# Kernel optimization log

Hardware: AMD Instinct MI355X
Metric: run time of the kernel (lower is better)

## Reference

```python
import jax, jax.numpy as jnp
import numpy as np

N = 100000        # nodes
E = 1_600_000     # edges (avg degree 16)
IN = 128          # in_feats
HID = 64          # hidden_feats
H = 3             # num_heads
OUT = 16          # out_feats
NEG_SLOPE = 0.2   # DGL GATConv default LeakyReLU slope


def setup_inputs() -> dict:
    key = jax.random.key(0)
    ks = jax.random.split(key, 16)
    f = lambda k, shape, s=0.1: (jax.random.normal(k, shape, jnp.float32) * s)
    return {
        "features": f(ks[0], (N, IN), 1.0),
        "src": jax.random.randint(ks[1], (E,), 0, N),
        "dst": jax.random.randint(ks[2], (E,), 0, N),
        # GATConv 1: in -> (H, HID)
        "W1": f(ks[3], (IN, H * HID)),
        "al1": f(ks[4], (H, HID)),
        "ar1": f(ks[5], (H, HID)),
        "b1": f(ks[6], (H, HID)),
        # GATConv 2: H*HID -> (H, HID)
        "W2": f(ks[7], (H * HID, H * HID)),
        "al2": f(ks[8], (H, HID)),
        "ar2": f(ks[9], (H, HID)),
        "b2": f(ks[10], (H, HID)),
        # MLP head
        "w3": f(ks[11], (H * HID, HID)),
        "b3": f(ks[12], (HID,)),
        "w4": f(ks[13], (HID, OUT)),
        "b4": f(ks[14], (OUT,)),
    }


def gat_layer(x, src, dst, W, al, ar, b):
    # feat: (N, H, D) projected features
    feat = (x @ W).reshape(-1, H, HID)
    el = jnp.einsum('nhd,hd->nh', feat, al)   # (N, H)
    er = jnp.einsum('nhd,hd->nh', feat, ar)   # (N, H)
    e = el[src] + er[dst]                     # (E, H) edge scores
    e = jnp.where(e > 0, e, NEG_SLOPE * e)    # LeakyReLU
    # numerically stable softmax over incoming edges of each dst node
    m = jax.lax.stop_gradient(jax.ops.segment_max(e, dst, num_segments=N))
    ex = jnp.exp(e - m[dst])
    s = jax.ops.segment_sum(ex, dst, num_segments=N)
    alpha = ex / s[dst]                       # (E, H)
    # message passing: scatter alpha-weighted src features to dst
    out = jax.ops.segment_sum(alpha[:, :, None] * feat[src], dst, num_segments=N)
    return jax.nn.relu(out + b)               # (N, H, D)


def reference(features, src, dst, W1, al1, ar1, b1, W2, al2, ar2, b2, w3, b3, w4, b4):
    x = gat_layer(features, src, dst, W1, al1, ar1, b1).reshape(N, H * HID)
    x = gat_layer(x, src, dst, W2, al2, ar2, b2).reshape(N, H * HID)
    h = jax.nn.relu(x @ w3 + b3)
    return h @ w4 + b4
```

## Files before the change

kernel.cpp:

```cpp
#include <hip/hip_runtime.h>
#include <cstdint>
#include <cstddef>

#define NN   100000
#define EE   1600000
#define INF_ 128
#define HIDF 64
#define NH   3
#define FEAT 192
#define OUTF 16
#define NEG  0.2f

#define NI4  25000
#define NB   98


__global__ void hist_kernel(const int* __restrict__ dst, int* __restrict__ counts) {
    int e = blockIdx.x * 256 + threadIdx.x;
    if (e < EE) atomicAdd(&counts[dst[e]], 1);
}

__global__ __launch_bounds__(256) void blocksum_kernel(const int* __restrict__ counts,
                                                       int* __restrict__ bsum) {
    int t = threadIdx.x;
    int idx4 = blockIdx.x * 256 + t;
    int s = 0;
    if (idx4 < NI4) {
        int4 v = ((const int4*)counts)[idx4];
        s = v.x + v.y + v.z + v.w;
    }
    __shared__ int sd[4];
    for (int o = 32; o; o >>= 1) s += __shfl_down(s, o, 64);
    if ((t & 63) == 0) sd[t >> 6] = s;
    __syncthreads();
    if (t == 0) bsum[blockIdx.x] = sd[0] + sd[1] + sd[2] + sd[3];
}

__global__ __launch_bounds__(128) void scanb_kernel(int* __restrict__ bsum) {
    __shared__ int sd[128];
    int t = threadIdx.x;
    int v = (t < NB) ? bsum[t] : 0;
    sd[t] = v;
    __syncthreads();
    for (int o = 1; o < 128; o <<= 1) {
        int u = (t >= o) ? sd[t - o] : 0;
        __syncthreads();
        sd[t] += u;
        __syncthreads();
    }
    if (t < NB) bsum[t] = sd[t] - v;
}

__global__ __launch_bounds__(256) void scanfinal_kernel(const int* __restrict__ counts,
                                                        const int* __restrict__ bsum,
                                                        int* __restrict__ row_ptr,
                                                        int* __restrict__ cursor) {
    __shared__ int sd[256];
    int t = threadIdx.x;
    int idx4 = blockIdx.x * 256 + t;
    int4 v = make_int4(0, 0, 0, 0);
    if (idx4 < NI4) v = ((const int4*)counts)[idx4];
    int s = v.x + v.y + v.z + v.w;
    sd[t] = s;
    __syncthreads();
    for (int o = 1; o < 256; o <<= 1) {
        int u = (t >= o) ? sd[t - o] : 0;
        __syncthreads();
        sd[t] += u;
        __syncthreads();
    }
    int base = bsum[blockIdx.x] + sd[t] - s;
    if (idx4 < NI4) {
        int4 r;
        r.x = base;
        r.y = base + v.x;
        r.z = base + v.x + v.y;
        r.w = base + v.x + v.y + v.z;
        ((int4*)row_ptr)[idx4] = r;
        ((int4*)cursor)[idx4]  = r;
    }
    if (blockIdx.x == 0 && t == 0) row_ptr[NN] = EE;
}

__global__ void scatter_kernel(const int* __restrict__ src, const int* __restrict__ dst,
                               int* __restrict__ cursor, int* __restrict__ ssrc) {
    int e = blockIdx.x * 256 + threadIdx.x;
    if (e < EE) {
        int p = atomicAdd(&cursor[dst[e]], 1);
        ssrc[p] = src[e];
    }
}


template <int K, int N, bool BIAS, bool RELU, bool ELER>
__global__ __launch_bounds__(256) void gemm64_kernel(const float* __restrict__ A,
                                                     const float* __restrict__ B,
                                                     const float* __restrict__ bias,
                                                     float* __restrict__ C,
                                                     const float* __restrict__ al,
                                                     const float* __restrict__ ar,
                                                     float* __restrict__ el,
                                                     float* __restrict__ er) {
    __shared__ float As[32][64];
    __shared__ float Bs[32][64];
    const int m0 = blockIdx.x * 64;
    const int n0 = blockIdx.y * 64;
    const int t  = threadIdx.x;
    const int tr = t >> 4;
    const int tc = t & 15;

    float acc[4][4] = {};

    for (int kt = 0; kt < K; kt += 32) {
        {
            int f = t;
#pragma unroll
            for (int it = 0; it < 2; ++it, f += 256) {
                int row = f >> 3, c4 = (f & 7) * 4;
                float4 v = make_float4(0.f, 0.f, 0.f, 0.f);
                int gr = m0 + row;
                if (gr < NN) v = *(const float4*)(A + (size_t)gr * K + kt + c4);
                As[c4 + 0][row] = v.x;
                As[c4 + 1][row] = v.y;
                As[c4 + 2][row] = v.z;
                As[c4 + 3][row] = v.w;
            }
        }
        {
            int f = t;
#pragma unroll
            for (int it = 0; it < 2; ++it, f += 256) {
                int row = f >> 4, c4 = (f & 15) * 4;
                *(float4*)&Bs[row][c4] = *(const float4*)(B + (size_t)(kt + row) * N + n0 + c4);
            }
        }
        __syncthreads();
#pragma unroll
        for (int k = 0; k < 32; ++k) {
            float4 a = *(const float4*)&As[k][tr * 4];
            float4 b = *(const float4*)&Bs[k][tc * 4];
            acc[0][0] += a.x * b.x; acc[0][1] += a.x * b.y; acc[0][2] += a.x * b.z; acc[0][3] += a.x * b.w;
            acc[1][0] += a.y * b.x; acc[1][1] += a.y * b.y; acc[1][2] += a.y * b.z; acc[1][3] += a.y * b.w;
            acc[2][0] += a.z * b.x; acc[2][1] += a.z * b.y; acc[2][2] += a.z * b.z; acc[2][3] += a.z * b.w;
            acc[3][0] += a.w * b.x; acc[3][1] += a.w * b.y; acc[3][2] += a.w * b.z; acc[3][3] += a.w * b.w;
        }
        __syncthreads();
    }

    float4 bv = make_float4(0.f, 0.f, 0.f, 0.f);
    if (BIAS) bv = *(const float4*)(bias + n0 + tc * 4);
#pragma unroll
    for (int i = 0; i < 4; ++i) {
        int row = m0 + tr * 4 + i;
        if (row >= NN) continue;
        float4 r;
        r.x = acc[i][0]; r.y = acc[i][1]; r.z = acc[i][2]; r.w = acc[i][3];
        if (BIAS) { r.x += bv.x; r.y += bv.y; r.z += bv.z; r.w += bv.w; }
        if (RELU) {
            r.x = fmaxf(r.x, 0.f); r.y = fmaxf(r.y, 0.f);
            r.z = fmaxf(r.z, 0.f); r.w = fmaxf(r.w, 0.f);
        }
        *(float4*)(C + (size_t)row * N + n0 + tc * 4) = r;
    }

    if (ELER) {
        const int h = blockIdx.y;
        float4 va = *(const float4*)(al + h * HIDF + tc * 4);
        float4 vb = *(const float4*)(ar + h * HIDF + tc * 4);
#pragma unroll
        for (int i = 0; i < 4; ++i) {
            float pl = acc[i][0] * va.x + acc[i][1] * va.y + acc[i][2] * va.z + acc[i][3] * va.w;
            float pr = acc[i][0] * vb.x + acc[i][1] * vb.y + acc[i][2] * vb.z + acc[i][3] * vb.w;
#pragma unroll
            for (int o = 1; o < 16; o <<= 1) {
                pl += __shfl_xor(pl, o, 16);
                pr += __shfl_xor(pr, o, 16);
            }
            int row = m0 + tr * 4 + i;
            if (tc == 0 && row < NN) {
                el[row * NH + h] = pl;
                er[row * NH + h] = pr;
            }
        }
    }
}


template <int K, int M, int ROWS, bool BIAS, bool RELU>
__global__ void rowgemm_kernel(const float* __restrict__ A, const float* __restrict__ W,
                               const float* __restrict__ bias, float* __restrict__ C) {
    __shared__ float a[ROWS][K];
    const int BT = M * ROWS;
    int r0 = blockIdx.x * ROWS;
    for (int i = threadIdx.x; i < ROWS * K; i += BT) {
        int rr = i / K, kk = i - rr * K;
        int row = r0 + rr;
        a[rr][kk] = (row < NN) ? A[(size_t)row * K + kk] : 0.f;
    }
    __syncthreads();
    int rr = threadIdx.x / M, c = threadIdx.x - rr * M;
    int row = r0 + rr;
    if (row >= NN) return;
    float acc = 0.f;
#pragma unroll
    for (int k = 0; k < K; ++k) acc += a[rr][k] * W[k * M + c];
    if (BIAS) acc += bias[c];
    if (RELU) acc = fmaxf(acc, 0.f);
    C[(size_t)row * M + c] = acc;
}


__global__ __launch_bounds__(256) void aggregate_kernel(
    const int* __restrict__ row_ptr, const int* __restrict__ ssrc,
    const float* __restrict__ feat, const float* __restrict__ el,
    const float* __restrict__ er, const float* __restrict__ bias,
    float* __restrict__ out) {
    int w = blockIdx.x * 4 + (threadIdx.x >> 6);
    if (w >= NN) return;
    int lane = threadIdx.x & 63;
    int beg = row_ptr[w], end = row_ptr[w + 1];
    float er0 = er[w * 3 + 0], er1 = er[w * 3 + 1], er2 = er[w * 3 + 2];

    float s0 = 0.f, s1 = 0.f, s2 = 0.f;
    float acc0 = 0.f, acc1 = 0.f, acc2 = 0.f;
    for (int e = beg; e < end; ++e) {
        int s = ssrc[e];
        float a0 = el[s * 3 + 0] + er0; a0 = a0 > 0.f ? a0 : NEG * a0;
        float a1 = el[s * 3 + 1] + er1; a1 = a1 > 0.f ? a1 : NEG * a1;
        float a2 = el[s * 3 + 2] + er2; a2 = a2 > 0.f ? a2 : NEG * a2;
        float w0 = __expf(a0), w1 = __expf(a1), w2 = __expf(a2);
        s0 += w0; s1 += w1; s2 += w2;
        const float* fr = feat + (size_t)s * FEAT;
        acc0 += w0 * fr[lane];
        acc1 += w1 * fr[64 + lane];
        acc2 += w2 * fr[128 + lane];
    }

    float r0, r1, r2;
    if (end > beg) { r0 = acc0 / s0; r1 = acc1 / s1; r2 = acc2 / s2; }
    else           { r0 = r1 = r2 = 0.f; }
    r0 += bias[lane]; r1 += bias[64 + lane]; r2 += bias[128 + lane];
    out[(size_t)w * FEAT + lane]       = fmaxf(r0, 0.f);
    out[(size_t)w * FEAT + 64 + lane]  = fmaxf(r1, 0.f);
    out[(size_t)w * FEAT + 128 + lane] = fmaxf(r2, 0.f);
}


extern "C" void kernel_launch(void* const* d_in, const int* in_sizes, int n_in,
                              void* d_out, int out_size, void* d_ws, size_t ws_size,
                              hipStream_t stream) {
    const float* features = (const float*)d_in[0];
    const int*   src      = (const int*)d_in[1];
    const int*   dst      = (const int*)d_in[2];
    const float* W1  = (const float*)d_in[3];
    const float* al1 = (const float*)d_in[4];
    const float* ar1 = (const float*)d_in[5];
    const float* b1  = (const float*)d_in[6];
    const float* W2  = (const float*)d_in[7];
    const float* al2 = (const float*)d_in[8];
    const float* ar2 = (const float*)d_in[9];
    const float* b2  = (const float*)d_in[10];
    const float* w3  = (const float*)d_in[11];
    const float* b3  = (const float*)d_in[12];
    const float* w4  = (const float*)d_in[13];
    const float* b4  = (const float*)d_in[14];
    float* out = (float*)d_out;

    char* p = (char*)d_ws;
    float* feat = (float*)p; p += (size_t)NN * FEAT * 4;
    float* x    = (float*)p; p += (size_t)NN * FEAT * 4;
    float* el   = (float*)p; p += (size_t)NN * NH * 4;
    float* er   = (float*)p; p += (size_t)NN * NH * 4;
    int* counts  = (int*)p;  p += (size_t)NN * 4;
    int* row_ptr = (int*)p;  p += (size_t)(NN + 4) * 4;
    int* cursor  = (int*)p;  p += (size_t)NN * 4;
    int* ssrc    = (int*)p;  p += (size_t)EE * 4;
    int* bsum    = (int*)p;  p += 128 * 4;

    const int GM = (NN + 63) / 64;

    hipMemsetAsync(counts, 0, (size_t)NN * 4, stream);
    hist_kernel<<<(EE + 255) / 256, 256, 0, stream>>>(dst, counts);
    blocksum_kernel<<<NB, 256, 0, stream>>>(counts, bsum);
    scanb_kernel<<<1, 128, 0, stream>>>(bsum);
    scanfinal_kernel<<<NB, 256, 0, stream>>>(counts, bsum, row_ptr, cursor);
    scatter_kernel<<<(EE + 255) / 256, 256, 0, stream>>>(src, dst, cursor, ssrc);

    gemm64_kernel<INF_, FEAT, false, false, true><<<dim3(GM, FEAT / 64), 256, 0, stream>>>(
        features, W1, nullptr, feat, al1, ar1, el, er);
    aggregate_kernel<<<(NN + 3) / 4, 256, 0, stream>>>(row_ptr, ssrc, feat, el, er, b1, x);

    gemm64_kernel<FEAT, FEAT, false, false, true><<<dim3(GM, FEAT / 64), 256, 0, stream>>>(
        x, W2, nullptr, feat, al2, ar2, el, er);
    aggregate_kernel<<<(NN + 3) / 4, 256, 0, stream>>>(row_ptr, ssrc, feat, el, er, b2, x);

    gemm64_kernel<FEAT, HIDF, true, true, false><<<dim3(GM, 1), 256, 0, stream>>>(
        x, w3, b3, feat, nullptr, nullptr, nullptr, nullptr);
    rowgemm_kernel<HIDF, OUTF, 16, true, false><<<NN / 16, 256, 0, stream>>>(feat, w4, b4, out);
}
```

Measured before the change: 944.7 us.

## Store intermediate node features and activations in bf16 to halve gather traffic

The projected features and aggregated activations are now stored as bf16 instead of fp32. GEMM epilogues convert to bf16 with rounding, and the GEMM A-loads and the aggregation gather convert bf16 back to fp32. The goal is to halve memory traffic in the gather-heavy aggregation and in the GEMM reads and writes. Accumulation stays in fp32, but the stored values lose precision, which may affect accuracy tolerance.

```diff
diff --git a/kernel.cpp b/kernel.cpp
--- a/kernel.cpp
+++ b/kernel.cpp
@@ -13,6 +13,17 @@
 
 #define NI4  25000
 #define NB   98
+
+typedef unsigned short ushort_t;
+typedef unsigned int   uint_t;
+
+__device__ __forceinline__ float bf2f(ushort_t u) {
+    return __uint_as_float(((uint_t)u) << 16);
+}
+__device__ __forceinline__ ushort_t f2bf(float f) {
+    uint_t b = __float_as_uint(f);
+    return (ushort_t)((b + 0x7FFFu + ((b >> 16) & 1u)) >> 16);
+}
 
 
 __global__ void hist_kernel(const int* __restrict__ dst, int* __restrict__ counts) {
@@ -92,11 +103,11 @@
 }
 
 
-template <int K, int N, bool BIAS, bool RELU, bool ELER>
-__global__ __launch_bounds__(256) void gemm64_kernel(const float* __restrict__ A,
+template <int K, int N, bool BIAS, bool RELU, bool ELER, bool A_BF16, bool C_BF16>
+__global__ __launch_bounds__(256) void gemm64_kernel(const void* __restrict__ Av,
                                                      const float* __restrict__ B,
                                                      const float* __restrict__ bias,
-                                                     float* __restrict__ C,
+                                                     void* __restrict__ Cv,
                                                      const float* __restrict__ al,
                                                      const float* __restrict__ ar,
                                                      float* __restrict__ el,
@@ -112,7 +123,26 @@
     float acc[4][4] = {};
 
     for (int kt = 0; kt < K; kt += 32) {
-        {
+        if (A_BF16) {
+            const ushort_t* A = (const ushort_t*)Av;
+            int row = t >> 2, c8 = (t & 3) * 8;
+            int gr = m0 + row;
+            if (gr < NN) {
+                uint4 v = *(const uint4*)(A + (size_t)gr * K + kt + c8);
+                As[c8 + 0][row] = bf2f((ushort_t)(v.x & 0xffff));
+                As[c8 + 1][row] = bf2f((ushort_t)(v.x >> 16));
+                As[c8 + 2][row] = bf2f((ushort_t)(v.y & 0xffff));
+                As[c8 + 3][row] = bf2f((ushort_t)(v.y >> 16));
+                As[c8 + 4][row] = bf2f((ushort_t)(v.z & 0xffff));
+                As[c8 + 5][row] = bf2f((ushort_t)(v.z >> 16));
+                As[c8 + 6][row] = bf2f((ushort_t)(v.w & 0xffff));
+                As[c8 + 7][row] = bf2f((ushort_t)(v.w >> 16));
+            } else {
+#pragma unroll
+                for (int j = 0; j < 8; ++j) As[c8 + j][row] = 0.f;
+            }
+        } else {
+            const float* A = (const float*)Av;
             int f = t;
 #pragma unroll
             for (int it = 0; it < 2; ++it, f += 256) {
@@ -160,7 +190,13 @@
             r.x = fmaxf(r.x, 0.f); r.y = fmaxf(r.y, 0.f);
             r.z = fmaxf(r.z, 0.f); r.w = fmaxf(r.w, 0.f);
         }
-        *(float4*)(C + (size_t)row * N + n0 + tc * 4) = r;
+        if (C_BF16) {
+            ushort4 u;
+            u.x = f2bf(r.x); u.y = f2bf(r.y); u.z = f2bf(r.z); u.w = f2bf(r.w);
+            *(ushort4*)((ushort_t*)Cv + (size_t)row * N + n0 + tc * 4) = u;
+        } else {
+            *(float4*)((float*)Cv + (size_t)row * N + n0 + tc * 4) = r;
+        }
     }
 
     if (ELER) {
@@ -212,9 +248,9 @@
 
 __global__ __launch_bounds__(256) void aggregate_kernel(
     const int* __restrict__ row_ptr, const int* __restrict__ ssrc,
-    const float* __restrict__ feat, const float* __restrict__ el,
+    const ushort_t* __restrict__ featb, const float* __restrict__ el,
     const float* __restrict__ er, const float* __restrict__ bias,
-    float* __restrict__ out) {
+    ushort_t* __restrict__ outb) {
     int w = blockIdx.x * 4 + (threadIdx.x >> 6);
     if (w >= NN) return;
     int lane = threadIdx.x & 63;
@@ -230,19 +266,19 @@
         float a2 = el[s * 3 + 2] + er2; a2 = a2 > 0.f ? a2 : NEG * a2;
         float w0 = __expf(a0), w1 = __expf(a1), w2 = __expf(a2);
         s0 += w0; s1 += w1; s2 += w2;
-        const float* fr = feat + (size_t)s * FEAT;
-        acc0 += w0 * fr[lane];
-        acc1 += w1 * fr[64 + lane];
-        acc2 += w2 * fr[128 + lane];
+        const ushort_t* fr = featb + (size_t)s * FEAT;
+        acc0 += w0 * bf2f(fr[lane]);
+        acc1 += w1 * bf2f(fr[64 + lane]);
+        acc2 += w2 * bf2f(fr[128 + lane]);
     }
 
     float r0, r1, r2;
     if (end > beg) { r0 = acc0 / s0; r1 = acc1 / s1; r2 = acc2 / s2; }
     else           { r0 = r1 = r2 = 0.f; }
     r0 += bias[lane]; r1 += bias[64 + lane]; r2 += bias[128 + lane];
-    out[(size_t)w * FEAT + lane]       = fmaxf(r0, 0.f);
-    out[(size_t)w * FEAT + 64 + lane]  = fmaxf(r1, 0.f);
-    out[(size_t)w * FEAT + 128 + lane] = fmaxf(r2, 0.f);
+    outb[(size_t)w * FEAT + lane]       = f2bf(fmaxf(r0, 0.f));
+    outb[(size_t)w * FEAT + 64 + lane]  = f2bf(fmaxf(r1, 0.f));
+    outb[(size_t)w * FEAT + 128 + lane] = f2bf(fmaxf(r2, 0.f));
 }
 
 
@@ -267,10 +303,11 @@
     float* out = (float*)d_out;
 
     char* p = (char*)d_ws;
-    float* feat = (float*)p; p += (size_t)NN * FEAT * 4;
-    float* x    = (float*)p; p += (size_t)NN * FEAT * 4;
-    float* el   = (float*)p; p += (size_t)NN * NH * 4;
-    float* er   = (float*)p; p += (size_t)NN * NH * 4;
+    ushort_t* featb = (ushort_t*)p; p += (size_t)NN * FEAT * 2;
+    ushort_t* xb    = (ushort_t*)p; p += (size_t)NN * FEAT * 2;
+    float* hid = (float*)p; p += (size_t)NN * HIDF * 4;
+    float* el  = (float*)p; p += (size_t)NN * NH * 4;
+    float* er  = (float*)p; p += (size_t)NN * NH * 4;
     int* counts  = (int*)p;  p += (size_t)NN * 4;
     int* row_ptr = (int*)p;  p += (size_t)(NN + 4) * 4;
     int* cursor  = (int*)p;  p += (size_t)NN * 4;
@@ -286,15 +323,15 @@
     scanfinal_kernel<<<NB, 256, 0, stream>>>(counts, bsum, row_ptr, cursor);
     scatter_kernel<<<(EE + 255) / 256, 256, 0, stream>>>(src, dst, cursor, ssrc);
 
-    gemm64_kernel<INF_, FEAT, false, false, true><<<dim3(GM, FEAT / 64), 256, 0, stream>>>(
-        features, W1, nullptr, feat, al1, ar1, el, er);
-    aggregate_kernel<<<(NN + 3) / 4, 256, 0, stream>>>(row_ptr, ssrc, feat, el, er, b1, x);
-
-    gemm64_kernel<FEAT, FEAT, false, false, true><<<dim3(GM, FEAT / 64), 256, 0, stream>>>(
-        x, W2, nullptr, feat, al2, ar2, el, er);
-    aggregate_kernel<<<(NN + 3) / 4, 256, 0, stream>>>(row_ptr, ssrc, feat, el, er, b2, x);
-
-    gemm64_kernel<FEAT, HIDF, true, true, false><<<dim3(GM, 1), 256, 0, stream>>>(
-        x, w3, b3, feat, nullptr, nullptr, nullptr, nullptr);
-    rowgemm_kernel<HIDF, OUTF, 16, true, false><<<NN / 16, 256, 0, stream>>>(feat, w4, b4, out);
-}
+    gemm64_kernel<INF_, FEAT, false, false, true, false, true>
+        <<<dim3(GM, FEAT / 64), 256, 0, stream>>>(features, W1, nullptr, featb, al1, ar1, el, er);
+    aggregate_kernel<<<(NN + 3) / 4, 256, 0, stream>>>(row_ptr, ssrc, featb, el, er, b1, xb);
+
+    gemm64_kernel<FEAT, FEAT, false, false, true, true, true>
+        <<<dim3(GM, FEAT / 64), 256, 0, stream>>>(xb, W2, nullptr, featb, al2, ar2, el, er);
+    aggregate_kernel<<<(NN + 3) / 4, 256, 0, stream>>>(row_ptr, ssrc, featb, el, er, b2, xb);
+
+    gemm64_kernel<FEAT, HIDF, true, true, false, true, false>
+        <<<dim3(GM, 1), 256, 0, stream>>>(xb, w3, b3, hid, nullptr, nullptr, nullptr, nullptr);
+    rowgemm_kernel<HIDF, OUTF, 16, true, false><<<NN / 16, 256, 0, stream>>>(hid, w4, b4, out);
+}
```

Measured after the change: 907.9 us. 1.04x faster.
